# Kernel optimization log

Measured on AMD Instinct MI355X. Metric: run time of the kernel, lower is better.

## Reference

```python
import jax, jax.numpy as jnp
import numpy as np

B, S, D_IN = 32, 4096, 256
D, T, NB, K = 256, 256, 4, 5  # d_model, compressed_len, n_blocks, kernel_size
EPS = 1e-5


def setup_inputs() -> dict:
    key = jax.random.key(0)
    ks = jax.random.split(key, 20)
    x = jax.random.normal(ks[0], (B, S, D_IN), jnp.float32)
    # ragged valid-prefix lengths in [1, S]
    lengths = jax.random.randint(ks[1], (B,), 1, S + 1)
    mask = jnp.arange(S)[None, :] < lengths[:, None]  # bool [B,S]
    sc = 0.02
    inp = {
        'x': x,
        'mask': mask,
        'in_w': jax.random.normal(ks[2], (D_IN, D), jnp.float32) * sc,
        'in_b': jnp.zeros((D,), jnp.float32),
        'ln_g': jnp.ones((NB, D), jnp.float32),
        'ln_b': jnp.zeros((NB, D), jnp.float32),
        'dw_w': jax.random.normal(ks[3], (NB, D, 1, K), jnp.float32) * sc,
        'dw_b': jnp.zeros((NB, D), jnp.float32),
        'win_w': jax.random.normal(ks[4], (NB, D, 2 * D), jnp.float32) * sc,
        'win_b': jnp.zeros((NB, 2 * D), jnp.float32),
        'wout_w': jax.random.normal(ks[5], (NB, D, D), jnp.float32) * sc,
        'wout_b': jnp.zeros((NB, D), jnp.float32),
        'fn_g': jnp.ones((D,), jnp.float32),
        'fn_b': jnp.zeros((D,), jnp.float32),
    }
    return inp


def layer_norm(h, g, b):
    mu = jnp.mean(h, axis=-1, keepdims=True)
    var = jnp.mean((h - mu) ** 2, axis=-1, keepdims=True)
    return (h - mu) * jax.lax.rsqrt(var + EPS) * g + b


def compress(x, mask, target_len):
    # Vectorized equivalent of the per-sample F.interpolate(mode='linear',
    # align_corners=False) loop: src = (j+0.5)*(L/T) - 0.5, clamped, lerp.
    lengths = mask.astype(jnp.int32).sum(axis=1)  # [B]
    Lf = lengths.astype(x.dtype)
    j = jnp.arange(target_len, dtype=x.dtype)
    src = (j[None, :] + 0.5) * (Lf[:, None] / target_len) - 0.5  # [B,T]
    src = jnp.clip(src, 0.0, jnp.maximum(Lf[:, None] - 1.0, 0.0))
    i0 = jnp.floor(src).astype(jnp.int32)
    i1 = jnp.minimum(i0 + 1, jnp.maximum(lengths[:, None] - 1, 0))
    w = (src - i0.astype(x.dtype))[..., None]  # [B,T,1]
    gather = jax.vmap(lambda xb, ib: xb[ib])  # [S,D],[T] -> [T,D]
    out = (1.0 - w) * gather(x, i0) + w * gather(x, i1)  # [B,T,D]
    valid = lengths > 0
    out = jnp.where(valid[:, None, None], out, 0.0)
    comp_mask = jnp.broadcast_to(valid[:, None], (x.shape[0], target_len))
    return out, comp_mask


def conv_block(h, g, b, dww, dwb, winw, winb, woutw, woutb):
    residual = h
    hn = layer_norm(h, g, b)
    hc = jax.lax.conv_general_dilated(
        hn.transpose(0, 2, 1), dww, window_strides=(1,),
        padding=[(K // 2, K // 2)], dimension_numbers=('NCW', 'OIW', 'NCW'),
        feature_group_count=D)
    hc = hc.transpose(0, 2, 1) + dwb  # [B,T,D]
    gv = hc @ winw + winb
    gate, val = jnp.split(gv, 2, axis=-1)
    h2 = jax.nn.sigmoid(gate) * jax.nn.gelu(val, approximate=False)
    return residual + h2 @ woutw + woutb


def reference(x, mask, in_w, in_b, ln_g, ln_b, dw_w, dw_b, win_w, win_b,
              wout_w, wout_b, fn_g, fn_b):
    xc, comp_mask = compress(x, mask, T)
    h = xc @ in_w + in_b
    for i in range(NB):
        h = conv_block(h, ln_g[i], ln_b[i], dw_w[i], dw_b[i], win_w[i],
                       win_b[i], wout_w[i], wout_b[i])
    return layer_norm(h, fn_g, fn_b), comp_mask
```

## Files before the change

kernel.cpp:

```cpp
#include <hip/hip_runtime.h>
#include <math.h>

#define B_    32
#define S_    4096
#define DIN_  256
#define D_    256
#define T_    256
#define NB_   4
#define K_    5
#define EPS_  1e-5f
#define ROWS_ (B_ * T_)

#define ORS_  16
#define CR_   32
#define BR_   36
#define SEGS_ 16
#define ASTR  264
#define HSTR  264

typedef short  shortx8 __attribute__((ext_vector_type(8)));
typedef float  floatx4 __attribute__((ext_vector_type(4)));

__device__ __forceinline__ unsigned short f2bf(float f) {
    unsigned int u = __float_as_uint(f);
    u += 0x7FFFu + ((u >> 16) & 1u);
    return (unsigned short)(u >> 16);
}
__device__ __forceinline__ float bf2f(unsigned short s) {
    return __uint_as_float((unsigned int)s << 16);
}
__device__ __forceinline__ unsigned int pack2bf(float a, float b) {
    return (unsigned int)f2bf(a) | ((unsigned int)f2bf(b) << 16);
}
__device__ __forceinline__ float bf2f_lo(unsigned int u) {
    return __uint_as_float(u << 16);
}
__device__ __forceinline__ float bf2f_hi(unsigned int u) {
    return __uint_as_float(u & 0xFFFF0000u);
}

__global__ void k_setup(const float* __restrict__ in_w, const float* __restrict__ win_w,
                        const float* __restrict__ wout_w, const unsigned int* __restrict__ mask_w,
                        unsigned short* __restrict__ wt_in, unsigned short* __restrict__ wt_in_lo,
                        unsigned short* __restrict__ wt_win,
                        unsigned short* __restrict__ wt_wout, int* __restrict__ lengths) {
    int z = blockIdx.z;
    int tid = threadIdx.x;

    if (z == 9) {
        int b = blockIdx.y * 16 + blockIdx.x;
        if (b >= B_) return;
        __shared__ int smode;
        if (tid < 64) {
            unsigned int w0 = mask_w[0];
            unsigned int vi = (tid < 32) ? mask_w[tid * 1024] : 0u;
            unsigned long long anyu8 = __ballot(vi > 1u);
            if (tid == 0) smode = (w0 == 0x3F800000u) ? 2 : (anyu8 ? 1 : 0);
        }
        __syncthreads();
        int mode = smode;
        int s = 0;
        if (mode == 0) {
            const int* m = (const int*)mask_w;
            for (int i = tid; i < S_; i += 256) s += (m[(size_t)b * S_ + i] != 0);
        } else if (mode == 2) {
            const float* m = (const float*)mask_w;
            for (int i = tid; i < S_; i += 256) s += (m[(size_t)b * S_ + i] != 0.0f);
        } else {
            const unsigned char* m = (const unsigned char*)mask_w;
            for (int i = tid; i < S_; i += 256) s += (m[(size_t)b * S_ + i] != 0);
        }
        __shared__ int sm[256];
        sm[tid] = s;
        __syncthreads();
        for (int off = 128; off > 0; off >>= 1) {
            if (tid < off) sm[tid] += sm[tid + off];
            __syncthreads();
        }
        if (tid == 0) lengths[b] = sm[0];
        return;
    }

    const float* src; unsigned short* dst; int N, Kd;
    if (z == 0)      { src = in_w;                                   dst = wt_in;                                   N = D_;     Kd = DIN_; }
    else if (z <= 4) { src = win_w  + (size_t)(z - 1) * D_ * 2 * D_; dst = wt_win  + (size_t)(z - 1) * 2 * D_ * D_; N = 2 * D_; Kd = D_; }
    else             { src = wout_w + (size_t)(z - 5) * D_ * D_;     dst = wt_wout + (size_t)(z - 5) * D_ * D_;     N = D_;     Kd = D_; }
    int bx = blockIdx.x * 32;
    int by = blockIdx.y * 32;
    if (bx >= N) return;
    __shared__ float tile[32][33];
    int tx = tid & 31, ty = tid >> 5;
#pragma unroll
    for (int i = 0; i < 32; i += 8)
        tile[ty + i][tx] = src[(size_t)(by + ty + i) * N + bx + tx];
    __syncthreads();
#pragma unroll
    for (int i = 0; i < 32; i += 8) {
        float f = tile[tx][ty + i];
        unsigned short h = f2bf(f);
        size_t idx = (size_t)(bx + ty + i) * Kd + by + tx;
        dst[idx] = h;
        if (z == 0) wt_in_lo[idx] = f2bf(f - bf2f(h));
    }
}

__global__ __launch_bounds__(512, 2) void k_fused(
    const float* __restrict__ x, const int* __restrict__ lengths,
    const unsigned short* __restrict__ wt_in, const unsigned short* __restrict__ wt_in_lo,
    const float* __restrict__ in_b,
    const float* __restrict__ ln_g, const float* __restrict__ ln_b,
    const float* __restrict__ dw_w, const float* __restrict__ dw_b,
    const unsigned short* __restrict__ wt_win, const float* __restrict__ win_b,
    const unsigned short* __restrict__ wt_wout, const float* __restrict__ wout_b,
    const float* __restrict__ fn_g, const float* __restrict__ fn_b,
    float* __restrict__ out0, float* __restrict__ out1)
{
    __shared__ unsigned short buf0[BR_][ASTR];
    __shared__ unsigned short buf1[CR_][ASTR];
    __shared__ float h_lds[CR_][HSTR];

    int tid = threadIdx.x;
    int w = tid >> 6, lane = tid & 63;
    int c16 = lane & 15, q = lane >> 4;
    int b = blockIdx.x >> 4, seg = blockIdx.x & (SEGS_ - 1);
    int t0 = seg * ORS_;

    unsigned short (*xlo)[ASTR] = (unsigned short (*)[ASTR])buf0;

    int L = lengths[b];

    {
        int tq = tid & 63, rg = tid >> 6;
        int col = tq * 4;
        float Lf = (float)L;
        float hi = fmaxf(Lf - 1.0f, 0.0f);
        int L1 = max(L - 1, 0);
        const float* xb = x + (size_t)b * S_ * DIN_ + col;
#pragma unroll
        for (int e = 0; e < 4; ++e) {
            int row = rg + e * 8;
            int t = t0 - 8 + row;
            t = min(max(t, 0), T_ - 1);
            float src = ((float)t + 0.5f) * (Lf * (1.0f / T_)) - 0.5f;
            src = fminf(fmaxf(src, 0.0f), hi);
            int i0 = (int)floorf(src);
            int i1 = min(i0 + 1, L1);
            float wf = src - (float)i0;
            float4 v0 = *(const float4*)&xb[(size_t)i0 * DIN_];
            float4 v1 = *(const float4*)&xb[(size_t)i1 * DIN_];
            float a0 = (1.0f - wf) * v0.x + wf * v1.x;
            float a1 = (1.0f - wf) * v0.y + wf * v1.y;
            float a2 = (1.0f - wf) * v0.z + wf * v1.z;
            float a3 = (1.0f - wf) * v0.w + wf * v1.w;
            unsigned short h0 = f2bf(a0), h1 = f2bf(a1), h2 = f2bf(a2), h3 = f2bf(a3);
            uint2 oh, ol;
            oh.x = (unsigned int)h0 | ((unsigned int)h1 << 16);
            oh.y = (unsigned int)h2 | ((unsigned int)h3 << 16);
            ol.x = (unsigned int)f2bf(a0 - bf2f(h0)) | ((unsigned int)f2bf(a1 - bf2f(h1)) << 16);
            ol.y = (unsigned int)f2bf(a2 - bf2f(h2)) | ((unsigned int)f2bf(a3 - bf2f(h3)) << 16);
            *(uint2*)&buf1[row][col] = oh;
            *(uint2*)&xlo[row][col] = ol;
        }
    }
    __syncthreads();

#pragma unroll
    for (int nn = 0; nn < 2; ++nn) {
        int nt = w + nn * 8;
        const unsigned short* wph = wt_in    + (size_t)(nt * 16 + c16) * 256 + q * 8;
        const unsigned short* wpl = wt_in_lo + (size_t)(nt * 16 + c16) * 256 + q * 8;
        floatx4 acc[2] = {};
#pragma unroll
        for (int kk = 0; kk < 8; ++kk) {
            shortx8 bh = *(const shortx8*)(wph + kk * 32);
            shortx8 bl = *(const shortx8*)(wpl + kk * 32);
#pragma unroll
            for (int mt = 0; mt < 2; ++mt) {
                shortx8 ah = *(const shortx8*)&buf1[mt * 16 + c16][kk * 32 + q * 8];
                shortx8 al = *(const shortx8*)&xlo[mt * 16 + c16][kk * 32 + q * 8];
                acc[mt] = __builtin_amdgcn_mfma_f32_16x16x32_bf16(ah, bh, acc[mt], 0, 0, 0);
                acc[mt] = __builtin_amdgcn_mfma_f32_16x16x32_bf16(al, bh, acc[mt], 0, 0, 0);
                acc[mt] = __builtin_amdgcn_mfma_f32_16x16x32_bf16(ah, bl, acc[mt], 0, 0, 0);
            }
        }
        float obv = in_b[nt * 16 + c16];
#pragma unroll
        for (int mt = 0; mt < 2; ++mt)
#pragma unroll
            for (int r = 0; r < 4; ++r)
                h_lds[mt * 16 + q * 4 + r][nt * 16 + c16] = acc[mt][r] + obv;
    }
    __syncthreads();

    if (tid < 132) {
        ((unsigned int*)buf0[0])[tid] = 0u;
        ((unsigned int*)buf0[1])[tid] = 0u;
        ((unsigned int*)buf0[BR_ - 2])[tid] = 0u;
        ((unsigned int*)buf0[BR_ - 1])[tid] = 0u;
    }

    for (int li = 0; li < NB_; ++li) {
        const float* g_i = ln_g + li * D_;
        const float* b_i = ln_b + li * D_;
        const float* dww = dw_w + (size_t)li * D_ * K_;
        const float* dwb = dw_b + li * D_;
        const unsigned short* ww = wt_win + (size_t)li * 2 * D_ * D_;
        const float* wb = win_b + (size_t)li * 2 * D_;
        const unsigned short* ow = wt_wout + (size_t)li * D_ * D_;
        const float* obp = wout_b + li * D_;

        shortx8 Bf[8];
        {
            const unsigned short* wp = ww + (size_t)(w * 16 + c16) * 256 + q * 8;
#pragma unroll
            for (int kk = 0; kk < 8; ++kk) Bf[kk] = *(const shortx8*)(wp + kk * 32);
        }

        {
            int c4 = lane * 4;
            float4 g4 = *(const float4*)&g_i[c4];
            float4 b4 = *(const float4*)&b_i[c4];
#pragma unroll
            for (int it = 0; it < 4; ++it) {
                int r = w + it * 8;
                float4 v = *(const float4*)&h_lds[r][c4];
                float s  = v.x + v.y + v.z + v.w;
                float ss = v.x * v.x + v.y * v.y + v.z * v.z + v.w * v.w;
#pragma unroll
                for (int off = 1; off < 64; off <<= 1) {
                    s += __shfl_xor(s, off);
                    ss += __shfl_xor(ss, off);
                }
                float mu = s * (1.0f / D_);
                float rsig = rsqrtf(ss * (1.0f / D_) - mu * mu + EPS_);
                uint2 o;
                o.x = pack2bf((v.x - mu) * rsig * g4.x + b4.x,
                              (v.y - mu) * rsig * g4.y + b4.y);
                o.y = pack2bf((v.z - mu) * rsig * g4.z + b4.z,
                              (v.w - mu) * rsig * g4.w + b4.w);
                int t = t0 - 8 + r;
                if (t < 0 || t >= T_) { o.x = 0; o.y = 0; }
                *(uint2*)&buf0[r + 2][c4] = o;
            }
        }
        __syncthreads();

        {
            int tq = tid & 63, rg = tid >> 6;
            int col = tq * 4;
            float4 wk[K_];
#pragma unroll
            for (int k = 0; k < K_; ++k) {
                wk[k].x = dww[(col + 0) * K_ + k];
                wk[k].y = dww[(col + 1) * K_ + k];
                wk[k].z = dww[(col + 2) * K_ + k];
                wk[k].w = dww[(col + 3) * K_ + k];
            }
            float4 cb4 = *(const float4*)&dwb[col];
#pragma unroll
            for (int e = 0; e < 4; ++e) {
                int rr = rg + e * 8;
                float4 acc = cb4;
#pragma unroll
                for (int k = 0; k < K_; ++k) {
                    uint2 u = *(const uint2*)&buf0[rr + k][col];
                    acc.x += bf2f_lo(u.x) * wk[k].x;
                    acc.y += bf2f_hi(u.x) * wk[k].y;
                    acc.z += bf2f_lo(u.y) * wk[k].z;
                    acc.w += bf2f_hi(u.y) * wk[k].w;
                }
                uint2 o;
                o.x = pack2bf(acc.x, acc.y);
                o.y = pack2bf(acc.z, acc.w);
                *(uint2*)&buf1[rr][col] = o;
            }
        }
        __syncthreads();

        float gvreg[2][2][4];
#pragma unroll
        for (int nn = 0; nn < 4; ++nn) {
            shortx8 Bn[8];
            {
                const unsigned short* wp = (nn < 3)
                    ? ww + (size_t)((w + (nn + 1) * 8) * 16 + c16) * 256 + q * 8
                    : ow + (size_t)(w * 16 + c16) * 256 + q * 8;
#pragma unroll
                for (int kk = 0; kk < 8; ++kk) Bn[kk] = *(const shortx8*)(wp + kk * 32);
            }
            floatx4 acc[2] = {};
#pragma unroll
            for (int kk = 0; kk < 8; ++kk)
#pragma unroll
                for (int mt = 0; mt < 2; ++mt) {
                    shortx8 a = *(const shortx8*)&buf1[mt * 16 + c16][kk * 32 + q * 8];
                    acc[mt] = __builtin_amdgcn_mfma_f32_16x16x32_bf16(a, Bf[kk], acc[mt], 0, 0, 0);
                }
            float bb = wb[(w + nn * 8) * 16 + c16];
            if (nn < 2) {
#pragma unroll
                for (int mt = 0; mt < 2; ++mt)
#pragma unroll
                    for (int r = 0; r < 4; ++r) gvreg[nn][mt][r] = acc[mt][r] + bb;
            } else {
                int pp = nn - 2;
                int colw = (w + pp * 8) * 16 + c16;
#pragma unroll
                for (int mt = 0; mt < 2; ++mt)
#pragma unroll
                    for (int r = 0; r < 4; ++r) {
                        float gate = gvreg[pp][mt][r];
                        float val  = acc[mt][r] + bb;
                        float sg = 1.0f / (1.0f + __expf(-gate));
                        float u = 1.5957691216f * (val + 0.044715f * val * val * val);
                        float ge = val / (1.0f + __expf(-u));
                        buf0[2 + mt * 16 + q * 4 + r][colw] = f2bf(sg * ge);
                    }
            }
#pragma unroll
            for (int kk = 0; kk < 8; ++kk) Bf[kk] = Bn[kk];
        }
        __syncthreads();

#pragma unroll
        for (int nn = 0; nn < 2; ++nn) {
            int nt = w + nn * 8;
            shortx8 Bn[8];
            if (nn == 0) {
                const unsigned short* wp = ow + (size_t)((w + 8) * 16 + c16) * 256 + q * 8;
#pragma unroll
                for (int kk = 0; kk < 8; ++kk) Bn[kk] = *(const shortx8*)(wp + kk * 32);
            }
            floatx4 acc[2] = {};
#pragma unroll
            for (int kk = 0; kk < 8; ++kk)
#pragma unroll
                for (int mt = 0; mt < 2; ++mt) {
                    shortx8 a = *(const shortx8*)&buf0[2 + mt * 16 + c16][kk * 32 + q * 8];
                    acc[mt] = __builtin_amdgcn_mfma_f32_16x16x32_bf16(a, Bf[kk], acc[mt], 0, 0, 0);
                }
            float bb = obp[nt * 16 + c16];
#pragma unroll
            for (int mt = 0; mt < 2; ++mt)
#pragma unroll
                for (int r = 0; r < 4; ++r) {
                    int row = mt * 16 + q * 4 + r;
                    int col = nt * 16 + c16;
                    h_lds[row][col] = h_lds[row][col] + acc[mt][r] + bb;
                }
            if (nn == 0) {
#pragma unroll
                for (int kk = 0; kk < 8; ++kk) Bf[kk] = Bn[kk];
            }
        }
        __syncthreads();
    }

    {
        int c4 = lane * 4;
        float4 g4 = *(const float4*)&fn_g[c4];
        float4 b4 = *(const float4*)&fn_b[c4];
#pragma unroll
        for (int it = 0; it < 2; ++it) {
            int r = 8 + w + it * 8;
            float4 v = *(const float4*)&h_lds[r][c4];
            float s  = v.x + v.y + v.z + v.w;
            float ss = v.x * v.x + v.y * v.y + v.z * v.z + v.w * v.w;
#pragma unroll
            for (int off = 1; off < 64; off <<= 1) {
                s += __shfl_xor(s, off);
                ss += __shfl_xor(ss, off);
            }
            float mu = s * (1.0f / D_);
            float rsig = rsqrtf(ss * (1.0f / D_) - mu * mu + EPS_);
            float4 o;
            o.x = (v.x - mu) * rsig * g4.x + b4.x;
            o.y = (v.y - mu) * rsig * g4.y + b4.y;
            o.z = (v.z - mu) * rsig * g4.z + b4.z;
            o.w = (v.w - mu) * rsig * g4.w + b4.w;
            *(float4*)&out0[((size_t)b * T_ + t0 + r - 8) * D_ + c4] = o;
        }
        if (tid < ORS_) out1[(size_t)b * T_ + t0 + tid] = 1.0f;
    }
}

extern "C" void kernel_launch(void* const* d_in, const int* in_sizes, int n_in,
                              void* d_out, int out_size, void* d_ws, size_t ws_size,
                              hipStream_t stream) {
    const float* x      = (const float*)d_in[0];
    const unsigned int* mask_w = (const unsigned int*)d_in[1];
    const float* in_w   = (const float*)d_in[2];
    const float* in_b   = (const float*)d_in[3];
    const float* ln_g   = (const float*)d_in[4];
    const float* ln_b   = (const float*)d_in[5];
    const float* dw_w   = (const float*)d_in[6];
    const float* dw_b   = (const float*)d_in[7];
    const float* win_w  = (const float*)d_in[8];
    const float* win_b  = (const float*)d_in[9];
    const float* wout_w = (const float*)d_in[10];
    const float* wout_b = (const float*)d_in[11];
    const float* fn_g   = (const float*)d_in[12];
    const float* fn_b   = (const float*)d_in[13];

    char* w8 = (char*)d_ws;
    unsigned short* wt_in   = (unsigned short*)w8;
    unsigned short* wt_win  = wt_in  + (size_t)D_ * DIN_;
    unsigned short* wt_wout = wt_win + (size_t)NB_ * 2 * D_ * D_;
    int* lengths = (int*)(w8 + (2u << 20));
    unsigned short* wt_in_lo = (unsigned short*)(w8 + (3u << 20));

    float* out0 = (float*)d_out;
    float* out1 = out0 + (size_t)ROWS_ * D_;

    k_setup<<<dim3(16, 8, 10), 256, 0, stream>>>(in_w, win_w, wout_w, mask_w,
                                                 wt_in, wt_in_lo, wt_win, wt_wout, lengths);
    k_fused<<<B_ * SEGS_, 512, 0, stream>>>(x, lengths, wt_in, wt_in_lo, in_b,
                                            ln_g, ln_b, dw_w, dw_b,
                                            wt_win, win_b, wt_wout, wout_b,
                                            fn_g, fn_b, out0, out1);
}
```

Measured before the change: 319.5 us.

## Switch block GEMMs to 32x32x16 MFMA tiles with per-wave 32-column ownership

Replaces the 16x16x32 MFMA tiling of the gate/value and output projections with 32x32x16 MFMA instructions. Each wave now computes a 32-row by 32-column tile of gate and value together, so the GLU activation no longer needs gate results held across iterations. The A-fragment LDS reads are shared between the gate and value MFMAs. The explicit software prefetch of weight fragments into registers is dropped; weights are loaded from global memory inside the k-loop, which may expose load latency in exchange for lower register pressure and fewer LDS reads.

```diff
diff --git a/kernel.cpp b/kernel.cpp
--- a/kernel.cpp
+++ b/kernel.cpp
@@ -18,8 +18,9 @@
 #define ASTR  264
 #define HSTR  264
 
-typedef short  shortx8 __attribute__((ext_vector_type(8)));
-typedef float  floatx4 __attribute__((ext_vector_type(4)));
+typedef short  shortx8  __attribute__((ext_vector_type(8)));
+typedef float  floatx4  __attribute__((ext_vector_type(4)));
+typedef float  floatx16 __attribute__((ext_vector_type(16)));
 
 __device__ __forceinline__ unsigned short f2bf(float f) {
     unsigned int u = __float_as_uint(f);
@@ -122,6 +123,7 @@
     int tid = threadIdx.x;
     int w = tid >> 6, lane = tid & 63;
     int c16 = lane & 15, q = lane >> 4;
+    int l31 = lane & 31, lh = lane >> 5;
     int b = blockIdx.x >> 4, seg = blockIdx.x & (SEGS_ - 1);
     int t0 = seg * ORS_;
 
@@ -209,13 +211,6 @@
         const unsigned short* ow = wt_wout + (size_t)li * D_ * D_;
         const float* obp = wout_b + li * D_;
 
-        shortx8 Bf[8];
-        {
-            const unsigned short* wp = ww + (size_t)(w * 16 + c16) * 256 + q * 8;
-#pragma unroll
-            for (int kk = 0; kk < 8; ++kk) Bf[kk] = *(const shortx8*)(wp + kk * 32);
-        }
-
         {
             int c4 = lane * 4;
             float4 g4 = *(const float4*)&g_i[c4];
@@ -277,80 +272,48 @@
         }
         __syncthreads();
 
-        float gvreg[2][2][4];
-#pragma unroll
-        for (int nn = 0; nn < 4; ++nn) {
-            shortx8 Bn[8];
-            {
-                const unsigned short* wp = (nn < 3)
-                    ? ww + (size_t)((w + (nn + 1) * 8) * 16 + c16) * 256 + q * 8
-                    : ow + (size_t)(w * 16 + c16) * 256 + q * 8;
-#pragma unroll
-                for (int kk = 0; kk < 8; ++kk) Bn[kk] = *(const shortx8*)(wp + kk * 32);
-            }
-            floatx4 acc[2] = {};
-#pragma unroll
-            for (int kk = 0; kk < 8; ++kk)
-#pragma unroll
-                for (int mt = 0; mt < 2; ++mt) {
-                    shortx8 a = *(const shortx8*)&buf1[mt * 16 + c16][kk * 32 + q * 8];
-                    acc[mt] = __builtin_amdgcn_mfma_f32_16x16x32_bf16(a, Bf[kk], acc[mt], 0, 0, 0);
-                }
-            float bb = wb[(w + nn * 8) * 16 + c16];
-            if (nn < 2) {
-#pragma unroll
-                for (int mt = 0; mt < 2; ++mt)
-#pragma unroll
-                    for (int r = 0; r < 4; ++r) gvreg[nn][mt][r] = acc[mt][r] + bb;
-            } else {
-                int pp = nn - 2;
-                int colw = (w + pp * 8) * 16 + c16;
-#pragma unroll
-                for (int mt = 0; mt < 2; ++mt)
-#pragma unroll
-                    for (int r = 0; r < 4; ++r) {
-                        float gate = gvreg[pp][mt][r];
-                        float val  = acc[mt][r] + bb;
-                        float sg = 1.0f / (1.0f + __expf(-gate));
-                        float u = 1.5957691216f * (val + 0.044715f * val * val * val);
-                        float ge = val / (1.0f + __expf(-u));
-                        buf0[2 + mt * 16 + q * 4 + r][colw] = f2bf(sg * ge);
-                    }
-            }
-#pragma unroll
-            for (int kk = 0; kk < 8; ++kk) Bf[kk] = Bn[kk];
-        }
-        __syncthreads();
-
-#pragma unroll
-        for (int nn = 0; nn < 2; ++nn) {
-            int nt = w + nn * 8;
-            shortx8 Bn[8];
-            if (nn == 0) {
-                const unsigned short* wp = ow + (size_t)((w + 8) * 16 + c16) * 256 + q * 8;
-#pragma unroll
-                for (int kk = 0; kk < 8; ++kk) Bn[kk] = *(const shortx8*)(wp + kk * 32);
-            }
-            floatx4 acc[2] = {};
-#pragma unroll
-            for (int kk = 0; kk < 8; ++kk)
-#pragma unroll
-                for (int mt = 0; mt < 2; ++mt) {
-                    shortx8 a = *(const shortx8*)&buf0[2 + mt * 16 + c16][kk * 32 + q * 8];
-                    acc[mt] = __builtin_amdgcn_mfma_f32_16x16x32_bf16(a, Bf[kk], acc[mt], 0, 0, 0);
-                }
-            float bb = obp[nt * 16 + c16];
-#pragma unroll
-            for (int mt = 0; mt < 2; ++mt)
-#pragma unroll
-                for (int r = 0; r < 4; ++r) {
-                    int row = mt * 16 + q * 4 + r;
-                    int col = nt * 16 + c16;
-                    h_lds[row][col] = h_lds[row][col] + acc[mt][r] + bb;
-                }
-            if (nn == 0) {
-#pragma unroll
-                for (int kk = 0; kk < 8; ++kk) Bf[kk] = Bn[kk];
+        {
+            floatx16 accG = {}, accV = {};
+            const unsigned short* wgp = ww + (size_t)(w * 32 + l31) * 256 + lh * 8;
+            const unsigned short* wvp = ww + (size_t)(256 + w * 32 + l31) * 256 + lh * 8;
+#pragma unroll
+            for (int kk = 0; kk < 16; ++kk) {
+                shortx8 a  = *(const shortx8*)&buf1[l31][kk * 16 + lh * 8];
+                shortx8 bg = *(const shortx8*)(wgp + kk * 16);
+                shortx8 bv = *(const shortx8*)(wvp + kk * 16);
+                accG = __builtin_amdgcn_mfma_f32_32x32x16_bf16(a, bg, accG, 0, 0, 0);
+                accV = __builtin_amdgcn_mfma_f32_32x32x16_bf16(a, bv, accV, 0, 0, 0);
+            }
+            float bg0 = wb[w * 32 + l31];
+            float bv0 = wb[256 + w * 32 + l31];
+#pragma unroll
+            for (int r = 0; r < 16; ++r) {
+                int row = (r & 3) + 8 * (r >> 2) + 4 * lh;
+                float gate = accG[r] + bg0;
+                float val  = accV[r] + bv0;
+                float sg = 1.0f / (1.0f + __expf(-gate));
+                float u = 1.5957691216f * (val + 0.044715f * val * val * val);
+                float ge = val / (1.0f + __expf(-u));
+                buf0[2 + row][w * 32 + l31] = f2bf(sg * ge);
+            }
+        }
+        __syncthreads();
+
+        {
+            floatx16 acc = {};
+            const unsigned short* wop = ow + (size_t)(w * 32 + l31) * 256 + lh * 8;
+#pragma unroll
+            for (int kk = 0; kk < 16; ++kk) {
+                shortx8 a  = *(const shortx8*)&buf0[2 + l31][kk * 16 + lh * 8];
+                shortx8 bo = *(const shortx8*)(wop + kk * 16);
+                acc = __builtin_amdgcn_mfma_f32_32x32x16_bf16(a, bo, acc, 0, 0, 0);
+            }
+            float bb = obp[w * 32 + l31];
+#pragma unroll
+            for (int r = 0; r < 16; ++r) {
+                int row = (r & 3) + 8 * (r >> 2) + 4 * lh;
+                int col = w * 32 + l31;
+                h_lds[row][col] = h_lds[row][col] + acc[r] + bb;
             }
         }
         __syncthreads();
```

Measured after the change: 315.1 us. About the same (-1.4%).
